# Kernel tuning notes

Hardware: AMD Instinct MI355X
Metric: run time of the kernel (lower is better)

The kernel has to match this reference:

```python
import jax, jax.numpy as jnp
import numpy as np

E = 32                       # early_it: number of leading K-dims used for the stats test
BOUND = -2.053748910631823   # norm.ppf(0.02)


def setup_inputs() -> dict:
    key = jax.random.key(0)
    k1, k2, k3 = jax.random.split(key, 3)
    B, S, H, OUT = 2, 2048, 2048, 8192
    x = jax.random.normal(k1, (B, S, H), dtype=jnp.float32)
    weight = jax.random.normal(k2, (OUT, H), dtype=jnp.float32) * (1.0 / np.sqrt(H))
    bias = jax.random.normal(k3, (OUT,), dtype=jnp.float32) * 0.02
    stats_w = jnp.ones((), dtype=jnp.float32)
    stats_b = jnp.zeros((), dtype=jnp.float32)
    return {"x": x, "weight": weight, "bias": bias, "stats_w": stats_w, "stats_b": stats_b}


def reference(x, weight, bias, stats_w, stats_b):
    B, S, H = x.shape
    OUT = weight.shape[0]
    x2 = x.reshape(B * S, H)           # [N, H]
    x_e, x_t = x2[:, :E], x2[:, E:]    # [N, E], [N, H-E]
    w_e, w_t = weight[:, :E], weight[:, E:]

    # partial GEMM over the first E dims + running sum of squares
    y1 = x_e @ w_e.T + bias[None, :]                 # [N, OUT]
    cum_sq = (x_e * x_e) @ (w_e * w_e).T             # [N, OUT]

    # exact stats test (torch_stats_test_ref_exact)
    n = jnp.float32(E)
    cur_mean = (y1 / n) * stats_w + stats_b
    cur_var = (cum_sq / n - cur_mean * cur_mean) * stats_w * stats_w
    test_stats = cur_mean / jnp.sqrt(cur_var / n)
    passed = test_stats < BOUND                      # [N, OUT] bool

    # remaining partial GEMM, then masked combine
    y2 = x_t @ w_t.T
    y = jnp.where(passed, jnp.zeros_like(y1), y1 + y2)
    return y.reshape(B, S, OUT)
```

## Files before the change

kernel.cpp:

```cpp
#include <hip/hip_runtime.h>
#include <hip/hip_bf16.h>
#include <hip/hip_fp16.h>
#include <stdint.h>

#define M_DIM 4096
#define K_DIM 2048
#define N_DIM 8192

typedef __attribute__((ext_vector_type(4))) float f32x4;
typedef __attribute__((ext_vector_type(8))) _Float16 f16x8;

typedef __attribute__((address_space(1))) const unsigned int g_u32_t;
typedef __attribute__((address_space(3))) unsigned int lds_u32_t;

static __device__ __forceinline__ void gload16(const void* g, void* l) {
  __builtin_amdgcn_global_load_lds((g_u32_t*)g, (lds_u32_t*)l, 16, 0, 0);
}

#define BOUNDF ((float)(-2.053748910631823))

__device__ __forceinline__ unsigned char gate_passed(float y1v, float sqv,
                                                     float sw, float sb) {
  float cm = y1v / 32.0f * sw + sb;
  float cmsq = cm * cm;
  asm volatile("" : "+v"(cmsq));
  float cv = (sqv / 32.0f - cmsq) * sw * sw;
  float ts = cm / sqrtf(cv / 32.0f);
  return (ts < BOUNDF) ? (unsigned char)1 : (unsigned char)0;
}

__global__ void cvt_f16_fused_kernel(const float* __restrict__ x,
                                     const float* __restrict__ wgt,
                                     unsigned short* __restrict__ xf,
                                     unsigned short* __restrict__ wf,
                                     float* __restrict__ xe,
                                     float* __restrict__ we,
                                     int n4x, int n4tot) {
  int i = blockIdx.x * blockDim.x + threadIdx.x;
  int stride = gridDim.x * blockDim.x;
  for (; i < n4tot; i += stride) {
    const float* src;
    unsigned short* dst;
    float* pe;
    int idx;
    if (i < n4x) {
      src = x; dst = xf; pe = xe; idx = i;
    } else {
      src = wgt; dst = wf; pe = we; idx = i - n4x;
    }
    float4 v = reinterpret_cast<const float4*>(src)[idx];
    int col4 = idx & (K_DIM / 4 - 1);
    if (col4 < 8) {
      int row = idx >> 9;
      reinterpret_cast<float4*>(pe)[row * 8 + col4] = v;
    }
    float xs[4] = {v.x, v.y, v.z, v.w};
    unsigned short hb[4];
#pragma unroll
    for (int j = 0; j < 4; ++j) {
      _Float16 h = (_Float16)xs[j];
      hb[j] = *reinterpret_cast<unsigned short*>(&h);
    }
    reinterpret_cast<ushort4*>(dst)[idx] = make_ushort4(hb[0], hb[1], hb[2], hb[3]);
  }
}

__global__ __launch_bounds__(256, 2) void mask_kernel(
    const float* __restrict__ xe_packed, const float* __restrict__ we_packed,
    const float* __restrict__ bias, const float* __restrict__ swp,
    const float* __restrict__ sbp, unsigned char* __restrict__ mask) {
  __shared__ __align__(16) unsigned char smem_bytes[128 * 36 * 4 + 32 * 128 * 4];
  float* xe_lds = (float*)smem_bytes;
  float* we_lds = (float*)(smem_bytes + 128 * 36 * 4);

  int row0 = blockIdx.x * 128, col0 = blockIdx.y * 128;
  int t = threadIdx.x, lane = t & 63, w = t >> 6;
  int wrow = (w >> 1) * 64, wcol = (w & 1) * 64;
  int cl = lane & 15, rg = lane >> 4;

#pragma unroll
  for (int it = 0; it < 4; ++it) {
    int idx = it * 256 + t;
    int r = idx >> 3, q = idx & 7;
    float4 v = reinterpret_cast<const float4*>(xe_packed)[(size_t)(row0 + r) * 8 + q];
    *reinterpret_cast<float4*>(&xe_lds[r * 36 + q * 4]) = v;
  }
#pragma unroll
  for (int it = 0; it < 4; ++it) {
    int idx = it * 256 + t;
    int c = idx & 127, kq = idx >> 7;
    float4 v = reinterpret_cast<const float4*>(we_packed)[(size_t)(col0 + c) * 8 + kq];
    we_lds[(kq * 4 + 0) * 128 + c] = v.x;
    we_lds[(kq * 4 + 1) * 128 + c] = v.y;
    we_lds[(kq * 4 + 2) * 128 + c] = v.z;
    we_lds[(kq * 4 + 3) * 128 + c] = v.w;
  }
  __syncthreads();

  float sw = *swp, sb = *sbp;

  float y1[16][4], sq[16][4];
#pragma unroll
  for (int r = 0; r < 16; ++r)
#pragma unroll
    for (int n = 0; n < 4; ++n) { y1[r][n] = 0.0f; sq[r][n] = 0.0f; }

#pragma unroll 2
  for (int k = 0; k < 32; ++k) {
    float wv[4], wv2[4];
#pragma unroll
    for (int n = 0; n < 4; ++n) {
      wv[n] = we_lds[k * 128 + wcol + n * 16 + cl];
      wv2[n] = wv[n] * wv[n];
    }
#pragma unroll
    for (int m = 0; m < 4; ++m) {
#pragma unroll
      for (int j = 0; j < 4; ++j) {
        float xv = xe_lds[(wrow + m * 16 + rg * 4 + j) * 36 + k];
        float xv2 = xv * xv;
#pragma unroll
        for (int n = 0; n < 4; ++n) {
          y1[m * 4 + j][n] = fmaf(xv, wv[n], y1[m * 4 + j][n]);
          sq[m * 4 + j][n] = fmaf(xv2, wv2[n], sq[m * 4 + j][n]);
        }
      }
    }
  }

#pragma unroll
  for (int m = 0; m < 4; ++m) {
#pragma unroll
    for (int n = 0; n < 4; ++n) {
      int c = col0 + wcol + n * 16 + cl;
      float bv = bias[c];
#pragma unroll
      for (int j = 0; j < 4; ++j) {
        int r = row0 + wrow + m * 16 + rg * 4 + j;
        mask[(size_t)r * N_DIM + c] =
            gate_passed(y1[m * 4 + j][n] + bv, sq[m * 4 + j][n], sw, sb);
      }
    }
  }
}

__global__ __launch_bounds__(256, 2) void gemm_f16_kernel(
    const unsigned short* __restrict__ xf, const unsigned short* __restrict__ wf,
    const float* __restrict__ bias, const unsigned char* __restrict__ mask,
    float* __restrict__ out) {
  __shared__ __align__(16) unsigned short smem[2 * 4096];

  int bid = blockIdx.x;
  int sid = (bid & 7) * 256 + (bid >> 3);
  int bm = sid >> 6;
  int bn = sid & 63;
  int row0 = bm * 128, col0 = bn * 128;

  int t = threadIdx.x, lane = t & 63, w = t >> 6;
  int wrow = (w >> 1) * 64, wcol = (w & 1) * 64;

  int Lr[2], Lg[2];
#pragma unroll
  for (int i = 0; i < 2; ++i) {
    int L = (w * 2 + i) * 1024 + lane * 16;
    int row = L >> 6;
    int s = (L >> 4) & 3;
    Lr[i] = row;
    Lg[i] = s ^ ((row >> 1) & 3);
  }

  int aoff[4], boff[4];
  int g = lane >> 4;
#pragma unroll
  for (int m = 0; m < 4; ++m) {
    int row = wrow + m * 16 + (lane & 15);
    aoff[m] = row * 32 + ((g ^ ((row >> 1) & 3)) * 8);
  }
#pragma unroll
  for (int n = 0; n < 4; ++n) {
    int row = wcol + n * 16 + (lane & 15);
    boff[n] = row * 32 + ((g ^ ((row >> 1) & 3)) * 8);
  }

  f32x4 acc[4][4];
#pragma unroll
  for (int m = 0; m < 4; ++m)
#pragma unroll
    for (int n = 0; n < 4; ++n) acc[m][n] = (f32x4){0.0f, 0.0f, 0.0f, 0.0f};

  const unsigned short* gpa0 = xf + (size_t)(row0 + Lr[0]) * K_DIM + Lg[0] * 8;
  const unsigned short* gpa1 = xf + (size_t)(row0 + Lr[1]) * K_DIM + Lg[1] * 8;
  const unsigned short* gpb0 = wf + (size_t)(col0 + Lr[0]) * K_DIM + Lg[0] * 8;
  const unsigned short* gpb1 = wf + (size_t)(col0 + Lr[1]) * K_DIM + Lg[1] * 8;
  char* lpa0 = (char*)smem + (w * 2 + 0) * 1024;
  char* lpa1 = (char*)smem + (w * 2 + 1) * 1024;
  char* lpb0 = lpa0 + 8192;
  char* lpb1 = lpa1 + 8192;

#pragma unroll 1
  for (int kt = 0; kt < K_DIM / 32; ++kt) {
    gload16(gpa0, lpa0);
    gload16(gpa1, lpa1);
    gload16(gpb0, lpb0);
    gload16(gpb1, lpb1);
    gpa0 += 32; gpa1 += 32; gpb0 += 32; gpb1 += 32;
    __syncthreads();

    f16x8 a[4], b[4];
#pragma unroll
    for (int m = 0; m < 4; ++m)
      a[m] = *reinterpret_cast<const f16x8*>(&smem[0 * 4096 + aoff[m]]);
#pragma unroll
    for (int n = 0; n < 4; ++n)
      b[n] = *reinterpret_cast<const f16x8*>(&smem[1 * 4096 + boff[n]]);
#pragma unroll
    for (int m = 0; m < 4; ++m)
#pragma unroll
      for (int n = 0; n < 4; ++n)
        acc[m][n] = __builtin_amdgcn_mfma_f32_16x16x32_f16(a[m], b[n], acc[m][n], 0, 0, 0);
    __syncthreads();
  }

  int cl = lane & 15, rg = lane >> 4;
#pragma unroll
  for (int m = 0; m < 4; ++m) {
    int rb = row0 + wrow + m * 16 + rg * 4;
#pragma unroll
    for (int n = 0; n < 4; ++n) {
      int c = col0 + wcol + n * 16 + cl;
      float bv = bias[c];
#pragma unroll
      for (int j = 0; j < 4; ++j) {
        size_t idx = (size_t)(rb + j) * N_DIM + c;
        out[idx] = mask[idx] ? 0.0f : (acc[m][n][j] + bv);
      }
    }
  }
}

__device__ __forceinline__ void stats4x4(const float* __restrict__ x,
                                         const float* __restrict__ w,
                                         int r0, int c0,
                                         float (&y1)[4][4], float (&sq)[4][4]) {
#pragma unroll
  for (int i = 0; i < 4; ++i)
#pragma unroll
    for (int j = 0; j < 4; ++j) { y1[i][j] = 0.0f; sq[i][j] = 0.0f; }
#pragma unroll
  for (int kc = 0; kc < 8; ++kc) {
    float4 xa[4], wa[4], x2[4], w2[4];
#pragma unroll
    for (int i = 0; i < 4; ++i)
      xa[i] = *reinterpret_cast<const float4*>(x + (size_t)(r0 + i) * K_DIM + kc * 4);
#pragma unroll
    for (int j = 0; j < 4; ++j)
      wa[j] = *reinterpret_cast<const float4*>(w + (size_t)(c0 + j) * K_DIM + kc * 4);
#pragma unroll
    for (int i = 0; i < 4; ++i)
      x2[i] = make_float4(xa[i].x * xa[i].x, xa[i].y * xa[i].y,
                          xa[i].z * xa[i].z, xa[i].w * xa[i].w);
#pragma unroll
    for (int j = 0; j < 4; ++j)
      w2[j] = make_float4(wa[j].x * wa[j].x, wa[j].y * wa[j].y,
                          wa[j].z * wa[j].z, wa[j].w * wa[j].w);
#pragma unroll
    for (int i = 0; i < 4; ++i)
#pragma unroll
      for (int j = 0; j < 4; ++j) {
        float a = y1[i][j];
        a = fmaf(xa[i].x, wa[j].x, a);
        a = fmaf(xa[i].y, wa[j].y, a);
        a = fmaf(xa[i].z, wa[j].z, a);
        a = fmaf(xa[i].w, wa[j].w, a);
        y1[i][j] = a;
        float b = sq[i][j];
        b = fmaf(x2[i].x, w2[j].x, b);
        b = fmaf(x2[i].y, w2[j].y, b);
        b = fmaf(x2[i].z, w2[j].z, b);
        b = fmaf(x2[i].w, w2[j].w, b);
        sq[i][j] = b;
      }
  }
}

__global__ void fallback_gemm_kernel(const float* __restrict__ x, const float* __restrict__ wgt,
                                     const float* __restrict__ bias, const float* __restrict__ swp,
                                     const float* __restrict__ sbp, float* __restrict__ out) {
  __shared__ float xs[64][36], ws2[64][36];
  int t = threadIdx.x;
  int tr = t >> 4, tc = t & 15;
  int r0 = blockIdx.x * 64, c0 = blockIdx.y * 64;
  float acc[4][4];
#pragma unroll
  for (int i = 0; i < 4; ++i)
#pragma unroll
    for (int j = 0; j < 4; ++j) acc[i][j] = 0.0f;

#pragma unroll 1
  for (int kt = 0; kt < K_DIM / 32; ++kt) {
#pragma unroll
    for (int i = 0; i < 2; ++i) {
      int idx = t + 256 * i;
      int row = idx >> 3;
      int kk = (idx & 7) * 4;
      *reinterpret_cast<float4*>(&xs[row][kk]) =
          *reinterpret_cast<const float4*>(x + (size_t)(r0 + row) * K_DIM + kt * 32 + kk);
      *reinterpret_cast<float4*>(&ws2[row][kk]) =
          *reinterpret_cast<const float4*>(wgt + (size_t)(c0 + row) * K_DIM + kt * 32 + kk);
    }
    __syncthreads();
#pragma unroll 4
    for (int k = 0; k < 32; ++k) {
      float xv[4], wv[4];
#pragma unroll
      for (int i = 0; i < 4; ++i) { xv[i] = xs[tr * 4 + i][k]; wv[i] = ws2[tc * 4 + i][k]; }
#pragma unroll
      for (int i = 0; i < 4; ++i)
#pragma unroll
        for (int j = 0; j < 4; ++j) acc[i][j] = fmaf(xv[i], wv[j], acc[i][j]);
    }
    __syncthreads();
  }

  float y1[4][4], sq[4][4];
  stats4x4(x, wgt, r0 + tr * 4, c0 + tc * 4, y1, sq);
  float sw = *swp, sb = *sbp;
#pragma unroll
  for (int i = 0; i < 4; ++i)
#pragma unroll
    for (int j = 0; j < 4; ++j) {
      int r = r0 + tr * 4 + i, c = c0 + tc * 4 + j;
      float bv = bias[c];
      unsigned char p = gate_passed(y1[i][j] + bv, sq[i][j], sw, sb);
      out[(size_t)r * N_DIM + c] = p ? 0.0f : (acc[i][j] + bv);
    }
}

extern "C" void kernel_launch(void* const* d_in, const int* in_sizes, int n_in,
                              void* d_out, int out_size, void* d_ws, size_t ws_size,
                              hipStream_t stream) {
  (void)in_sizes; (void)n_in; (void)out_size;
  const float* x    = (const float*)d_in[0];
  const float* wgt  = (const float*)d_in[1];
  const float* bias = (const float*)d_in[2];
  const float* swp  = (const float*)d_in[3];
  const float* sbp  = (const float*)d_in[4];
  float* out = (float*)d_out;

  const size_t xf_off = 0;
  const size_t wf_off = xf_off + (size_t)M_DIM * K_DIM * 2;
  const size_t xe_off = wf_off + (size_t)N_DIM * K_DIM * 2;
  const size_t we_off = xe_off + (size_t)M_DIM * 32 * 4;
  const size_t mk_off = we_off + (size_t)N_DIM * 32 * 4;
  const size_t need   = mk_off + (size_t)M_DIM * N_DIM;

  if (ws_size >= need) {
    unsigned short* xf = (unsigned short*)((char*)d_ws + xf_off);
    unsigned short* wf = (unsigned short*)((char*)d_ws + wf_off);
    float* xe = (float*)((char*)d_ws + xe_off);
    float* we = (float*)((char*)d_ws + we_off);
    unsigned char* mk  = (unsigned char*)((char*)d_ws + mk_off);

    int n4x = M_DIM * K_DIM / 4;
    int n4tot = n4x + N_DIM * K_DIM / 4;
    hipLaunchKernelGGL(cvt_f16_fused_kernel, dim3(2048), dim3(256), 0, stream,
                       x, wgt, xf, wf, xe, we, n4x, n4tot);
    hipLaunchKernelGGL(mask_kernel, dim3(M_DIM / 128, N_DIM / 128), dim3(256), 0, stream,
                       xe, we, bias, swp, sbp, mk);
    hipLaunchKernelGGL(gemm_f16_kernel, dim3(2048), dim3(256), 0, stream,
                       xf, wf, bias, mk, out);
  } else {
    hipLaunchKernelGGL(fallback_gemm_kernel, dim3(M_DIM / 64, N_DIM / 64), dim3(256), 0, stream,
                       x, wgt, bias, swp, sbp, out);
  }
}
```

Measured before the change: 309.1 us.

## Vectorize mask-kernel LDS reads with row-major W tile; remap GEMM block swizzle

The mask kernel now stores the weight tile row-major with the same padded stride as the x tile. Both operands are read as float4 vectors over four K values per step, which replaces scalar LDS loads and the transposing scalar stores. The GEMM kernel's block-index mapping changes so that each XCD (bid & 7) covers a 16x16 tile region instead of a strided band, aiming for better L2 reuse of A and B per XCD. The risk is more LDS bank conflicts from strided float4 reads, and higher register pressure from the fully unrolled loop.

After: 300.0 us. 3.0% less time.

```diff
diff --git a/kernel.cpp b/kernel.cpp
--- a/kernel.cpp
+++ b/kernel.cpp
@@ -69,7 +69,7 @@
     const float* __restrict__ xe_packed, const float* __restrict__ we_packed,
     const float* __restrict__ bias, const float* __restrict__ swp,
     const float* __restrict__ sbp, unsigned char* __restrict__ mask) {
-  __shared__ __align__(16) unsigned char smem_bytes[128 * 36 * 4 + 32 * 128 * 4];
+  __shared__ __align__(16) unsigned char smem_bytes[2 * 128 * 36 * 4];
   float* xe_lds = (float*)smem_bytes;
   float* we_lds = (float*)(smem_bytes + 128 * 36 * 4);
 
@@ -82,18 +82,10 @@
   for (int it = 0; it < 4; ++it) {
     int idx = it * 256 + t;
     int r = idx >> 3, q = idx & 7;
-    float4 v = reinterpret_cast<const float4*>(xe_packed)[(size_t)(row0 + r) * 8 + q];
-    *reinterpret_cast<float4*>(&xe_lds[r * 36 + q * 4]) = v;
-  }
-#pragma unroll
-  for (int it = 0; it < 4; ++it) {
-    int idx = it * 256 + t;
-    int c = idx & 127, kq = idx >> 7;
-    float4 v = reinterpret_cast<const float4*>(we_packed)[(size_t)(col0 + c) * 8 + kq];
-    we_lds[(kq * 4 + 0) * 128 + c] = v.x;
-    we_lds[(kq * 4 + 1) * 128 + c] = v.y;
-    we_lds[(kq * 4 + 2) * 128 + c] = v.z;
-    we_lds[(kq * 4 + 3) * 128 + c] = v.w;
+    *reinterpret_cast<float4*>(&xe_lds[r * 36 + q * 4]) =
+        reinterpret_cast<const float4*>(xe_packed)[(size_t)(row0 + r) * 8 + q];
+    *reinterpret_cast<float4*>(&we_lds[r * 36 + q * 4]) =
+        reinterpret_cast<const float4*>(we_packed)[(size_t)(col0 + r) * 8 + q];
   }
   __syncthreads();
 
@@ -105,24 +97,29 @@
 #pragma unroll
     for (int n = 0; n < 4; ++n) { y1[r][n] = 0.0f; sq[r][n] = 0.0f; }
 
-#pragma unroll 2
-  for (int k = 0; k < 32; ++k) {
-    float wv[4], wv2[4];
+#pragma unroll
+  for (int kq = 0; kq < 8; ++kq) {
+    f32x4 wv4[4], wvsq[4];
 #pragma unroll
     for (int n = 0; n < 4; ++n) {
-      wv[n] = we_lds[k * 128 + wcol + n * 16 + cl];
-      wv2[n] = wv[n] * wv[n];
+      wv4[n] = *reinterpret_cast<const f32x4*>(&we_lds[(wcol + n * 16 + cl) * 36 + kq * 4]);
+      wvsq[n] = wv4[n] * wv4[n];
     }
 #pragma unroll
     for (int m = 0; m < 4; ++m) {
 #pragma unroll
       for (int j = 0; j < 4; ++j) {
-        float xv = xe_lds[(wrow + m * 16 + rg * 4 + j) * 36 + k];
-        float xv2 = xv * xv;
-#pragma unroll
-        for (int n = 0; n < 4; ++n) {
-          y1[m * 4 + j][n] = fmaf(xv, wv[n], y1[m * 4 + j][n]);
-          sq[m * 4 + j][n] = fmaf(xv2, wv2[n], sq[m * 4 + j][n]);
+        f32x4 xv4 = *reinterpret_cast<const f32x4*>(
+            &xe_lds[(wrow + m * 16 + rg * 4 + j) * 36 + kq * 4]);
+#pragma unroll
+        for (int kk = 0; kk < 4; ++kk) {
+          float xv = xv4[kk];
+          float xv2 = xv * xv;
+#pragma unroll
+          for (int n = 0; n < 4; ++n) {
+            y1[m * 4 + j][n] = fmaf(xv, wv4[n][kk], y1[m * 4 + j][n]);
+            sq[m * 4 + j][n] = fmaf(xv2, wvsq[n][kk], sq[m * 4 + j][n]);
+          }
         }
       }
     }
@@ -151,9 +148,9 @@
   __shared__ __align__(16) unsigned short smem[2 * 4096];
 
   int bid = blockIdx.x;
-  int sid = (bid & 7) * 256 + (bid >> 3);
-  int bm = sid >> 6;
-  int bn = sid & 63;
+  int xk = bid & 7, j = bid >> 3;
+  int bm = (xk & 1) * 16 + (j >> 4);
+  int bn = (xk >> 1) * 16 + (j & 15);
   int row0 = bm * 128, col0 = bn * 128;
 
   int t = threadIdx.x, lane = t & 63, w = t >> 6;
```
